# Performance work log

Measured on AMD Instinct MI355X. Metric: run time of the kernel, lower is better.

## Reference

```python
import jax, jax.numpy as jnp
import numpy as np

# ---- module hyperparameters (init_kwargs) ----
V0 = 1.0
SIGMA0 = 0.5
GAUSS_CONST = V0 / (np.sqrt(2.0 * np.pi) * SIGMA0)
NW, NF, D, H = 4096, 16, 3, 256  # walkers, fermions, dimensions, hidden width
N = NF * D


def setup_inputs() -> dict:
    key = jax.random.key(0)
    k0, k1, k2, k3 = jax.random.split(key, 4)
    sc = lambda k, shape, fan_in: jax.random.normal(k, shape, jnp.float32) / np.sqrt(fan_in).astype(np.float32)
    return {
        "x": jax.random.normal(k0, (NW, NF, D), jnp.float32),
        "W1": sc(k1, (N, H), N),
        "b1": jnp.zeros((H,), jnp.float32),
        "W2": sc(k2, (H, H), H),
        "b2": jnp.zeros((H,), jnp.float32),
        "w3": sc(k3, (H,), H),
        "b3": jnp.zeros((), jnp.float32),
    }


def _logpsi(xf, W1, b1, W2, b2, w3, b3):
    # xf: (N,) flattened single-walker coordinates -> scalar log|psi|
    h = jnp.tanh(xf @ W1 + b1)
    h = jnp.tanh(h @ W2 + b2)
    return h @ w3 + b3


def reference(x, W1, b1, W2, b2, w3, b3):
    nw, nf, d = x.shape
    xflat = x.reshape(nw, nf * d)

    f = lambda xf: _logpsi(xf, W1, b1, W2, b2, w3, b3)
    grad_f = jax.grad(f)

    def kinetic_one(xf):
        g = grad_f(xf)                      # (N,) d logpsi / dx
        hess = jax.jacfwd(grad_f)(xf)       # (N, N) forward-over-reverse Hessian
        lap = jnp.trace(hess)
        return -0.5 * (lap + jnp.sum(g * g))

    kin = jax.vmap(kinetic_one)(xflat)      # (nw,)

    # harmonic potential 1/2 sum x^2
    pot = 0.5 * jnp.sum(xflat * xflat, axis=1)

    # Gaussian interaction, faithful to source: unsqueeze(-2)/unsqueeze(-1) on
    # (nw, nf, d) broadcasts to (nw, nf, d, d) intra-particle coordinate diffs,
    # then sum over last axis -> (nw, nf, d), triu(k=1) over trailing (nf, d).
    diff = x[..., None, :] - x[..., :, None]            # (nw, nf, d, d)
    sqdist = jnp.sum(diff * diff, axis=-1)              # (nw, nf, d)
    mask = jnp.triu(jnp.ones((nf, d), x.dtype), k=1)    # (nf, d)
    inter = GAUSS_CONST * jnp.sum(jnp.exp(-sqdist / (2.0 * SIGMA0 ** 2)) * mask, axis=(-2, -1))

    eloc = kin + pot + inter
    return (eloc, kin, pot, inter)
```

## Files before the change

### kernel.cpp

```cpp
#include <hip/hip_runtime.h>
#include <cmath>

#define NWALK 4096
#define NXD   48
#define HID   256
#define WPB   8
#define GCONST 0.7978845608028654f

typedef _Float16 half8   __attribute__((ext_vector_type(8)));
typedef float    float4v __attribute__((ext_vector_type(4)));

__global__ __launch_bounds__(256) void prep_all(const float* __restrict__ W2,
                                                const float* __restrict__ W1,
                                                const float* __restrict__ x,
                                                const float* __restrict__ b1,
                                                _Float16* __restrict__ W2c,
                                                _Float16* __restrict__ W1c,
                                                _Float16* __restrict__ t1h,
                                                _Float16* __restrict__ h1h,
                                                _Float16* __restrict__ ch) {
    __shared__ float tile[64][65];
    __shared__ float xs[16][NXD];

    if (blockIdx.x < 16) {
        const int bi = blockIdx.x & 3;
        const int bj = blockIdx.x >> 2;
        const int tx = threadIdx.x & 63;
        const int ty = threadIdx.x >> 6;
        #pragma unroll
        for (int r = 0; r < 16; ++r) {
            int il = ty * 16 + r;
            tile[tx][il] = W2[(bi * 64 + il) * HID + bj * 64 + tx];
        }
        __syncthreads();
        #pragma unroll
        for (int r = 0; r < 16; ++r) {
            int jl = ty * 16 + r;
            W2c[(bj * 64 + jl) * HID + bi * 64 + tx] = (_Float16)tile[jl][tx];
        }
        #pragma unroll
        for (int r = 0; r < 3; ++r) {
            int k = blockIdx.x * 3 + r;
            W1c[k * HID + threadIdx.x] = (_Float16)W1[k * HID + threadIdx.x];
        }
    } else {
        const int i  = threadIdx.x;
        const int w0 = (blockIdx.x - 16) * 16;

        float col[NXD];
        float S = 0.f;
        #pragma unroll
        for (int k = 0; k < NXD; ++k) {
            float v = W1[k * HID + i];
            col[k] = v;
            S = fmaf(v, v, S);
        }
        #pragma unroll
        for (int t = threadIdx.x; t < 16 * NXD; t += 256)
            ((float*)xs)[t] = x[w0 * NXD + t];
        __syncthreads();

        const float b = b1[i];
        #pragma unroll 4
        for (int w = 0; w < 16; ++w) {
            float a1 = b;
            #pragma unroll
            for (int k = 0; k < NXD; ++k)
                a1 = fmaf(xs[w][k], col[k], a1);
            float h1 = tanhf(a1);
            float t1 = 1.f - h1 * h1;
            int off = (w0 + w) * HID + i;
            t1h[off] = (_Float16)t1;
            h1h[off] = (_Float16)h1;
            ch[off]  = (_Float16)(S * h1 * t1);
        }
    }
}

__global__ __launch_bounds__(256) void prep2(
    const float* __restrict__ b2, const float* __restrict__ w3,
    const _Float16* __restrict__ W2c,
    const _Float16* __restrict__ h1h, const _Float16* __restrict__ ch,
    float* __restrict__ uf, float* __restrict__ uhf, float* __restrict__ rt2g)
{
    __shared__ float b2s[HID], w3s[HID];
    __shared__ float r2s[4][8];

    const int tid  = threadIdx.x;
    const int wave = tid >> 6;
    const int lane = tid & 63;
    const int n16  = lane & 15;
    const int quad = lane >> 4;
    const int w0   = blockIdx.x * 8;

    b2s[tid] = b2[tid];
    w3s[tid] = w3[tid];

    half8 afr[8][4];
    #pragma unroll
    for (int s = 0; s < 8; ++s)
        #pragma unroll
        for (int a = 0; a < 4; ++a)
            afr[s][a] = *(const half8*)(W2c + ((wave * 4 + a) * 16 + n16) * HID
                                        + s * 32 + quad * 8);

    const _Float16* src  = (n16 & 1) ? ch : h1h;
    const _Float16* brow = src + (size_t)(w0 + (n16 >> 1)) * HID;

    float4v acc[4];
    #pragma unroll
    for (int a = 0; a < 4; ++a) acc[a] = (float4v){0.f, 0.f, 0.f, 0.f};
    #pragma unroll
    for (int s = 0; s < 8; ++s) {
        half8 bf = *(const half8*)(brow + (s * 4 + quad) * 8);
        #pragma unroll
        for (int a = 0; a < 4; ++a)
            acc[a] = __builtin_amdgcn_mfma_f32_16x16x32_f16(afr[s][a], bf, acc[a], 0, 0, 0);
    }

    __syncthreads();

    const int w = n16 >> 1;
    float um[4][4];
    #pragma unroll
    for (int a = 0; a < 4; ++a)
        #pragma unroll
        for (int reg = 0; reg < 4; ++reg) um[a][reg] = 0.f;

    if (!(n16 & 1)) {
        #pragma unroll
        for (int a = 0; a < 4; ++a)
            #pragma unroll
            for (int reg = 0; reg < 4; ++reg) {
                int i   = (wave * 4 + a) * 16 + quad * 4 + reg;
                float a2 = acc[a][reg] + b2s[i];
                float h2 = tanhf(a2);
                float t2 = 1.f - h2 * h2;
                float u  = w3s[i] * t2;
                um[a][reg] = u;
                uf [(size_t)(w0 + w) * HID + i] = u;
                uhf[(size_t)(w0 + w) * HID + i] = u * h2;
            }
    }

    float part = 0.f;
    #pragma unroll
    for (int a = 0; a < 4; ++a)
        #pragma unroll
        for (int reg = 0; reg < 4; ++reg) {
            float uo = __shfl_xor(um[a][reg], 1, 64);
            part = fmaf(uo, acc[a][reg], part);
        }
    part += __shfl_xor(part, 16, 64);
    part += __shfl_xor(part, 32, 64);
    if (quad == 0 && (n16 & 1)) r2s[wave][w] = part;
    __syncthreads();
    if (tid < 8)
        rt2g[w0 + tid] = r2s[0][tid] + r2s[1][tid] + r2s[2][tid] + r2s[3][tid];
}

__global__ __launch_bounds__(256, 2) void eloc8(
    const float* __restrict__ x,
    const _Float16* __restrict__ W2c,
    const _Float16* __restrict__ W1c,
    const _Float16* __restrict__ t1h,
    const float* __restrict__ uf,
    const float* __restrict__ uhf,
    const float* __restrict__ rt2g,
    float* __restrict__ out)
{
    __shared__ __align__(16) _Float16 AsT[2][48 * HID];
    __shared__ float xs[WPB][NXD];
    __shared__ float gw[WPB][4][NXD];
    __shared__ float rt1p[WPB][4][16];

    const int w0   = blockIdx.x * WPB;
    const int tid  = threadIdx.x;
    const int wave = tid >> 6;
    const int lane = tid & 63;
    const int n16  = lane & 15;
    const int quad = (tid >> 4) & 3;
    const int ci   = tid & 31;
    const int k0   = tid >> 5;

    half8 afr[8][4];
    #pragma unroll
    for (int s = 0; s < 8; ++s)
        #pragma unroll
        for (int a = 0; a < 4; ++a)
            afr[s][a] = *(const half8*)(W2c + ((wave * 4 + a) * 16 + n16) * HID
                                        + s * 32 + quad * 8);

    half8 w1r[6];
    #pragma unroll
    for (int s2 = 0; s2 < 6; ++s2)
        w1r[s2] = *(const half8*)(W1c + (s2 * 8 + k0) * HID + ci * 8);

    #pragma unroll
    for (int t = tid; t < WPB * NXD; t += 256)
        ((float*)xs)[t] = x[w0 * NXD + t];

    {
        half8 th = *(const half8*)(t1h + (size_t)w0 * HID + ci * 8);
        #pragma unroll
        for (int s2 = 0; s2 < 6; ++s2) {
            int k = s2 * 8 + k0;
            *(half8*)(AsT[0] + k * HID + ((ci ^ (k & 7)) * 8)) = w1r[s2] * th;
        }
    }
    __syncthreads();

    #pragma unroll 1
    for (int ww = 0; ww < WPB; ++ww) {
        const int cur = ww & 1, nxt = cur ^ 1;
        const int wg  = w0 + ww;
        const _Float16* curA = AsT[cur];
        const bool more = (ww + 1 < WPB);

        const int wn = more ? (wg + 1) : wg;
        half8 th = *(const half8*)(t1h + (size_t)wn * HID + ci * 8);

        const float* ub = uf  + (size_t)wg * HID + wave * 64 + quad * 4;
        const float* hb = uhf + (size_t)wg * HID + wave * 64 + quad * 4;
        float4v uu[4], uh[4];
        #pragma unroll
        for (int a = 0; a < 4; ++a) uu[a] = *(const float4v*)(ub + a * 16);
        #pragma unroll
        for (int a = 0; a < 4; ++a) uh[a] = *(const float4v*)(hb + a * 16);

        float rt1 = 0.f;
        #pragma unroll 1
        for (int kt = 0; kt < 3; ++kt) {
            float4v acc[4];
            #pragma unroll
            for (int a = 0; a < 4; ++a) acc[a] = (float4v){0.f, 0.f, 0.f, 0.f};
            const int krow = kt * 16 + n16;
            __builtin_amdgcn_s_setprio(1);
            #pragma unroll
            for (int s = 0; s < 8; ++s) {
                half8 bf = *(const half8*)(curA + krow * HID
                            + ((((s * 4 + quad) ^ (krow & 7)) << 3)));
                #pragma unroll
                for (int a = 0; a < 4; ++a)
                    acc[a] = __builtin_amdgcn_mfma_f32_16x16x32_f16(
                        afr[s][a], bf, acc[a], 0, 0, 0);
            }
            __builtin_amdgcn_s_setprio(0);
            float g = 0.f;
            #pragma unroll
            for (int a = 0; a < 4; ++a)
                #pragma unroll
                for (int reg = 0; reg < 4; ++reg) {
                    float m = acc[a][reg];
                    rt1 = fmaf(m * m, uh[a][reg], rt1);
                    g   = fmaf(m, uu[a][reg], g);
                }
            g += __shfl_xor(g, 16, 64);
            g += __shfl_xor(g, 32, 64);
            if (lane < 16) gw[ww][wave][kt * 16 + lane] = g;
        }

        rt1 += __shfl_xor(rt1, 16, 64);
        rt1 += __shfl_xor(rt1, 32, 64);
        if (lane < 16) rt1p[ww][wave][lane] = rt1;

        if (more) {
            #pragma unroll
            for (int s2 = 0; s2 < 6; ++s2) {
                int k = s2 * 8 + k0;
                *(half8*)(AsT[nxt] + k * HID + ((ci ^ (k & 7)) * 8)) = w1r[s2] * th;
            }
        }
        __syncthreads();
    }

    const int wa = 2 * wave, wb = wa + 1;
    float rt2a = rt2g[w0 + wa];
    float rt2b = rt2g[w0 + wb];

    float r0 = rt1p[wa][quad][n16];
    float r1 = rt1p[wb][quad][n16];

    float ga = 0.f, gb = 0.f, xa = 0.f, xb = 0.f;
    if (lane < NXD) {
        ga = gw[wa][0][lane] + gw[wa][1][lane] + gw[wa][2][lane] + gw[wa][3][lane];
        gb = gw[wb][0][lane] + gw[wb][1][lane] + gw[wb][2][lane] + gw[wb][3][lane];
        xa = xs[wa][lane];
        xb = xs[wb][lane];
    }
    float gga = ga * ga, ggb = gb * gb;
    float pa = 0.5f * xa * xa, pb = 0.5f * xb * xb;
    #pragma unroll
    for (int off = 32; off > 0; off >>= 1) {
        r0  += __shfl_down(r0,  off, 64);
        r1  += __shfl_down(r1,  off, 64);
        gga += __shfl_down(gga, off, 64);
        ggb += __shfl_down(ggb, off, 64);
        pa  += __shfl_down(pa,  off, 64);
        pb  += __shfl_down(pb,  off, 64);
    }
    if (lane == 0) {
        float kina = r0 + rt2a - 0.5f * gga;
        float kinb = r1 + rt2b - 0.5f * ggb;

        float x0 = xs[wa][0], x1 = xs[wa][1], x2 = xs[wa][2];
        float x3 = xs[wa][3], x4 = xs[wa][4], x5 = xs[wa][5];
        float d01 = (x0-x1)*(x0-x1) + (x2-x1)*(x2-x1);
        float d02 = (x0-x2)*(x0-x2) + (x1-x2)*(x1-x2);
        float d12 = (x3-x5)*(x3-x5) + (x4-x5)*(x4-x5);
        float intera = GCONST * (expf(-2.f*d01) + expf(-2.f*d02) + expf(-2.f*d12));

        x0 = xs[wb][0]; x1 = xs[wb][1]; x2 = xs[wb][2];
        x3 = xs[wb][3]; x4 = xs[wb][4]; x5 = xs[wb][5];
        float e01 = (x0-x1)*(x0-x1) + (x2-x1)*(x2-x1);
        float e02 = (x0-x2)*(x0-x2) + (x1-x2)*(x1-x2);
        float e12 = (x3-x5)*(x3-x5) + (x4-x5)*(x4-x5);
        float interb = GCONST * (expf(-2.f*e01) + expf(-2.f*e02) + expf(-2.f*e12));

        const int wga = w0 + wa, wgb = w0 + wb;
        out[wga]             = kina + pa + intera;
        out[NWALK + wga]     = kina;
        out[2 * NWALK + wga] = pa;
        out[3 * NWALK + wga] = intera;
        out[wgb]             = kinb + pb + interb;
        out[NWALK + wgb]     = kinb;
        out[2 * NWALK + wgb] = pb;
        out[3 * NWALK + wgb] = interb;
    }
}

extern "C" void kernel_launch(void* const* d_in, const int* in_sizes, int n_in,
                              void* d_out, int out_size, void* d_ws, size_t ws_size,
                              hipStream_t stream) {
    const float* x  = (const float*)d_in[0];
    const float* W1 = (const float*)d_in[1];
    const float* b1 = (const float*)d_in[2];
    const float* W2 = (const float*)d_in[3];
    const float* b2 = (const float*)d_in[4];
    const float* w3 = (const float*)d_in[5];
    float* out = (float*)d_out;

    char* ws = (char*)d_ws;
    _Float16* W2c = (_Float16*)(ws);
    _Float16* W1c = (_Float16*)(ws + 131072);
    _Float16* t1h = (_Float16*)(ws + 155648);
    _Float16* h1h = (_Float16*)(ws + 2252800);
    _Float16* chv = (_Float16*)(ws + 4349952);
    float*    uf  = (float*)(ws + 6447104);
    float*    uhf = (float*)(ws + 10641408);
    float*    r2g = (float*)(ws + 14835712);

    prep_all<<<16 + NWALK / 16, 256, 0, stream>>>(W2, W1, x, b1, W2c, W1c, t1h, h1h, chv);
    prep2<<<NWALK / 8, 256, 0, stream>>>(b2, w3, W2c, h1h, chv, uf, uhf, r2g);
    eloc8<<<NWALK / WPB, 256, 0, stream>>>(x, W2c, W1c, t1h, uf, uhf, r2g, out);
}
```

Before: 123.2 us.

## Fuse second-layer prep kernel into main Laplacian kernel and single-buffer LDS

After: 109.1 us. -11.5%, faster.

```diff
diff --git a/kernel.cpp b/kernel.cpp
--- a/kernel.cpp
+++ b/kernel.cpp
@@ -77,102 +77,25 @@
     }
 }
 
-__global__ __launch_bounds__(256) void prep2(
-    const float* __restrict__ b2, const float* __restrict__ w3,
-    const _Float16* __restrict__ W2c,
-    const _Float16* __restrict__ h1h, const _Float16* __restrict__ ch,
-    float* __restrict__ uf, float* __restrict__ uhf, float* __restrict__ rt2g)
-{
-    __shared__ float b2s[HID], w3s[HID];
-    __shared__ float r2s[4][8];
-
-    const int tid  = threadIdx.x;
-    const int wave = tid >> 6;
-    const int lane = tid & 63;
-    const int n16  = lane & 15;
-    const int quad = lane >> 4;
-    const int w0   = blockIdx.x * 8;
-
-    b2s[tid] = b2[tid];
-    w3s[tid] = w3[tid];
-
-    half8 afr[8][4];
-    #pragma unroll
-    for (int s = 0; s < 8; ++s)
-        #pragma unroll
-        for (int a = 0; a < 4; ++a)
-            afr[s][a] = *(const half8*)(W2c + ((wave * 4 + a) * 16 + n16) * HID
-                                        + s * 32 + quad * 8);
-
-    const _Float16* src  = (n16 & 1) ? ch : h1h;
-    const _Float16* brow = src + (size_t)(w0 + (n16 >> 1)) * HID;
-
-    float4v acc[4];
-    #pragma unroll
-    for (int a = 0; a < 4; ++a) acc[a] = (float4v){0.f, 0.f, 0.f, 0.f};
-    #pragma unroll
-    for (int s = 0; s < 8; ++s) {
-        half8 bf = *(const half8*)(brow + (s * 4 + quad) * 8);
-        #pragma unroll
-        for (int a = 0; a < 4; ++a)
-            acc[a] = __builtin_amdgcn_mfma_f32_16x16x32_f16(afr[s][a], bf, acc[a], 0, 0, 0);
-    }
-
-    __syncthreads();
-
-    const int w = n16 >> 1;
-    float um[4][4];
-    #pragma unroll
-    for (int a = 0; a < 4; ++a)
-        #pragma unroll
-        for (int reg = 0; reg < 4; ++reg) um[a][reg] = 0.f;
-
-    if (!(n16 & 1)) {
-        #pragma unroll
-        for (int a = 0; a < 4; ++a)
-            #pragma unroll
-            for (int reg = 0; reg < 4; ++reg) {
-                int i   = (wave * 4 + a) * 16 + quad * 4 + reg;
-                float a2 = acc[a][reg] + b2s[i];
-                float h2 = tanhf(a2);
-                float t2 = 1.f - h2 * h2;
-                float u  = w3s[i] * t2;
-                um[a][reg] = u;
-                uf [(size_t)(w0 + w) * HID + i] = u;
-                uhf[(size_t)(w0 + w) * HID + i] = u * h2;
-            }
-    }
-
-    float part = 0.f;
-    #pragma unroll
-    for (int a = 0; a < 4; ++a)
-        #pragma unroll
-        for (int reg = 0; reg < 4; ++reg) {
-            float uo = __shfl_xor(um[a][reg], 1, 64);
-            part = fmaf(uo, acc[a][reg], part);
-        }
-    part += __shfl_xor(part, 16, 64);
-    part += __shfl_xor(part, 32, 64);
-    if (quad == 0 && (n16 & 1)) r2s[wave][w] = part;
-    __syncthreads();
-    if (tid < 8)
-        rt2g[w0 + tid] = r2s[0][tid] + r2s[1][tid] + r2s[2][tid] + r2s[3][tid];
-}
-
 __global__ __launch_bounds__(256, 2) void eloc8(
     const float* __restrict__ x,
+    const float* __restrict__ b2,
+    const float* __restrict__ w3,
     const _Float16* __restrict__ W2c,
     const _Float16* __restrict__ W1c,
     const _Float16* __restrict__ t1h,
-    const float* __restrict__ uf,
-    const float* __restrict__ uhf,
-    const float* __restrict__ rt2g,
+    const _Float16* __restrict__ h1h,
+    const _Float16* __restrict__ ch,
     float* __restrict__ out)
 {
-    __shared__ __align__(16) _Float16 AsT[2][48 * HID];
+    __shared__ __align__(16) _Float16 AsT[48 * HID];
     __shared__ float xs[WPB][NXD];
     __shared__ float gw[WPB][4][NXD];
     __shared__ float rt1p[WPB][4][16];
+    __shared__ float us[WPB][HID], uhs[WPB][HID];
+    __shared__ float b2s[HID], w3s[HID];
+    __shared__ float r2s[4][WPB];
+    __shared__ float rt2s[WPB];
 
     const int w0   = blockIdx.x * WPB;
     const int tid  = threadIdx.x;
@@ -196,37 +119,91 @@
     for (int s2 = 0; s2 < 6; ++s2)
         w1r[s2] = *(const half8*)(W1c + (s2 * 8 + k0) * HID + ci * 8);
 
+    b2s[tid] = b2[tid];
+    w3s[tid] = w3[tid];
     #pragma unroll
     for (int t = tid; t < WPB * NXD; t += 256)
         ((float*)xs)[t] = x[w0 * NXD + t];
 
     {
-        half8 th = *(const half8*)(t1h + (size_t)w0 * HID + ci * 8);
+        const _Float16* src  = (n16 & 1) ? ch : h1h;
+        const _Float16* brow = src + (size_t)(w0 + (n16 >> 1)) * HID;
+
+        float4v acc[4];
+        #pragma unroll
+        for (int a = 0; a < 4; ++a) acc[a] = (float4v){0.f, 0.f, 0.f, 0.f};
+        #pragma unroll
+        for (int s = 0; s < 8; ++s) {
+            half8 bf = *(const half8*)(brow + (s * 4 + quad) * 8);
+            #pragma unroll
+            for (int a = 0; a < 4; ++a)
+                acc[a] = __builtin_amdgcn_mfma_f32_16x16x32_f16(afr[s][a], bf, acc[a], 0, 0, 0);
+        }
+
+        half8 th0 = *(const half8*)(t1h + (size_t)w0 * HID + ci * 8);
         #pragma unroll
         for (int s2 = 0; s2 < 6; ++s2) {
             int k = s2 * 8 + k0;
-            *(half8*)(AsT[0] + k * HID + ((ci ^ (k & 7)) * 8)) = w1r[s2] * th;
-        }
-    }
+            *(half8*)(AsT + k * HID + ((ci ^ (k & 7)) * 8)) = w1r[s2] * th0;
+        }
+
+        __syncthreads();
+
+        const int w = n16 >> 1;
+        float um[4][4];
+        #pragma unroll
+        for (int a = 0; a < 4; ++a)
+            #pragma unroll
+            for (int reg = 0; reg < 4; ++reg) um[a][reg] = 0.f;
+
+        if (!(n16 & 1)) {
+            #pragma unroll
+            for (int a = 0; a < 4; ++a)
+                #pragma unroll
+                for (int reg = 0; reg < 4; ++reg) {
+                    int i    = (wave * 4 + a) * 16 + quad * 4 + reg;
+                    float a2 = acc[a][reg] + b2s[i];
+                    float h2 = tanhf(a2);
+                    float t2 = 1.f - h2 * h2;
+                    float u  = w3s[i] * t2;
+                    um[a][reg] = u;
+                    us [w][i] = u;
+                    uhs[w][i] = u * h2;
+                }
+        }
+
+        float part = 0.f;
+        #pragma unroll
+        for (int a = 0; a < 4; ++a)
+            #pragma unroll
+            for (int reg = 0; reg < 4; ++reg) {
+                float uo = __shfl_xor(um[a][reg], 1, 64);
+                part = fmaf(uo, acc[a][reg], part);
+            }
+        part += __shfl_xor(part, 16, 64);
+        part += __shfl_xor(part, 32, 64);
+        if (quad == 0 && (n16 & 1)) r2s[wave][w] = part;
+    }
+    __syncthreads();
+    if (tid < WPB)
+        rt2s[tid] = r2s[0][tid] + r2s[1][tid] + r2s[2][tid] + r2s[3][tid];
     __syncthreads();
 
     #pragma unroll 1
     for (int ww = 0; ww < WPB; ++ww) {
-        const int cur = ww & 1, nxt = cur ^ 1;
-        const int wg  = w0 + ww;
-        const _Float16* curA = AsT[cur];
+        const int wg   = w0 + ww;
         const bool more = (ww + 1 < WPB);
 
         const int wn = more ? (wg + 1) : wg;
         half8 th = *(const half8*)(t1h + (size_t)wn * HID + ci * 8);
 
-        const float* ub = uf  + (size_t)wg * HID + wave * 64 + quad * 4;
-        const float* hb = uhf + (size_t)wg * HID + wave * 64 + quad * 4;
         float4v uu[4], uh[4];
         #pragma unroll
-        for (int a = 0; a < 4; ++a) uu[a] = *(const float4v*)(ub + a * 16);
-        #pragma unroll
-        for (int a = 0; a < 4; ++a) uh[a] = *(const float4v*)(hb + a * 16);
+        for (int a = 0; a < 4; ++a)
+            uu[a] = *(const float4v*)(&us[ww][(wave * 4 + a) * 16 + quad * 4]);
+        #pragma unroll
+        for (int a = 0; a < 4; ++a)
+            uh[a] = *(const float4v*)(&uhs[ww][(wave * 4 + a) * 16 + quad * 4]);
 
         float rt1 = 0.f;
         #pragma unroll 1
@@ -238,7 +215,7 @@
             __builtin_amdgcn_s_setprio(1);
             #pragma unroll
             for (int s = 0; s < 8; ++s) {
-                half8 bf = *(const half8*)(curA + krow * HID
+                half8 bf = *(const half8*)(AsT + krow * HID
                             + ((((s * 4 + quad) ^ (krow & 7)) << 3)));
                 #pragma unroll
                 for (int a = 0; a < 4; ++a)
@@ -264,19 +241,21 @@
         rt1 += __shfl_xor(rt1, 32, 64);
         if (lane < 16) rt1p[ww][wave][lane] = rt1;
 
+        __syncthreads();
+
         if (more) {
             #pragma unroll
             for (int s2 = 0; s2 < 6; ++s2) {
                 int k = s2 * 8 + k0;
-                *(half8*)(AsT[nxt] + k * HID + ((ci ^ (k & 7)) * 8)) = w1r[s2] * th;
+                *(half8*)(AsT + k * HID + ((ci ^ (k & 7)) * 8)) = w1r[s2] * th;
             }
         }
         __syncthreads();
     }
 
     const int wa = 2 * wave, wb = wa + 1;
-    float rt2a = rt2g[w0 + wa];
-    float rt2b = rt2g[w0 + wb];
+    float rt2a = rt2s[wa];
+    float rt2b = rt2s[wb];
 
     float r0 = rt1p[wa][quad][n16];
     float r1 = rt1p[wb][quad][n16];
@@ -346,11 +325,7 @@
     _Float16* t1h = (_Float16*)(ws + 155648);
     _Float16* h1h = (_Float16*)(ws + 2252800);
     _Float16* chv = (_Float16*)(ws + 4349952);
-    float*    uf  = (float*)(ws + 6447104);
-    float*    uhf = (float*)(ws + 10641408);
-    float*    r2g = (float*)(ws + 14835712);
 
     prep_all<<<16 + NWALK / 16, 256, 0, stream>>>(W2, W1, x, b1, W2c, W1c, t1h, h1h, chv);
-    prep2<<<NWALK / 8, 256, 0, stream>>>(b2, w3, W2c, h1h, chv, uf, uhf, r2g);
-    eloc8<<<NWALK / WPB, 256, 0, stream>>>(x, W2c, W1c, t1h, uf, uhf, r2g, out);
+    eloc8<<<NWALK / WPB, 256, 0, stream>>>(x, b2, w3, W2c, W1c, t1h, h1h, chv, out);
 }
```
